# Performance work log

Hardware: AMD Instinct MI355X
Metric: run time of the kernel (lower is better)

Reference implementation:

```python
import jax, jax.numpy as jnp
import numpy as np

EPS = 1e-5
KEEP_FRAC = 0.925


def conv1x1(x, w, b):
    # x: [B,C,H,W], w: [O,C], b: [O]
    return jnp.einsum('bchw,oc->bohw', x, w) + b[None, :, None, None]


def adain_norm(x):
    m = x.mean(axis=(2, 3), keepdims=True)
    v = x.var(axis=(2, 3), keepdims=True)
    return (x - m) / jnp.sqrt(v + EPS)


def zca_norm(x):
    B, C, H, W = x.shape
    f = x.reshape(B, C, H * W)
    m = f.mean(axis=-1, keepdims=True)
    fc = f - m
    cov = jnp.einsum('bcn,bdn->bcd', fc, fc) / (H * W - 1) + EPS * jnp.eye(C, dtype=x.dtype)
    s, U = jnp.linalg.eigh(cov)
    Ud = U * (1.0 / jnp.sqrt(s + EPS))[:, None, :]          # U @ diag(s^-1/2)
    whiten = jnp.einsum('bce,bde->bcd', Ud, U)              # U diag U^T
    out = jnp.einsum('bcd,bdn->bcn', whiten, fc)
    return out.reshape(B, C, H, W)


def correlation_block(xq, yk, wf, bf, wg, bg):
    B, C, H, W = xq.shape
    f = conv1x1(xq, wf, bf).reshape(B, C, -1)   # [B,C,n_x]
    g = conv1x1(yk, wg, bg).reshape(B, C, -1)   # [B,C,n_y]
    energy = jnp.einsum('bcn,bcm->bnm', f, g)   # f^T g : [B,n_x,n_y]
    corr = jax.nn.softmax(energy, axis=-1)
    atten = corr.mean(axis=1, keepdims=True)    # mean over n_x -> [B,1,n_y]
    return corr, atten


def attn_mask(a):
    # a: [B,1,n]; zero the positions of the k smallest values (union over batch, as in torch)
    n = a.shape[2]
    k = int(n * KEEP_FRAC)
    idx = jnp.argsort(a, axis=2)[:, :, :k]                   # smallest k per (b, channel)
    mask = jnp.ones_like(a).at[:, :, idx.reshape(-1)].set(0.0)
    return mask


def corr_mask(mx, my):
    # mx: [B,1,n_x], my: [B,1,n_y] -> equality mask [B,n_x,n_y]
    return (mx[:, 0, :, None] == my[:, 0, None, :]).astype(mx.dtype)


def savanet_forward(x, y, f_w, f_b, g_w, g_b, sa_f_w, sa_f_b, sa_g_w, sa_g_b, h_w, h_b, out_w, out_b):
    B, C, H, W = x.shape
    n = H * W
    x_adain = adain_norm(x)
    y_adain = adain_norm(y)
    x_zca = zca_norm(x)
    y_zca = zca_norm(y)
    correlation, _ = correlation_block(x_adain, y_adain, f_w, f_b, g_w, g_b)
    _, atten_x = correlation_block(x_zca, x_zca, sa_f_w, sa_f_b, sa_g_w, sa_g_b)
    _, atten_y = correlation_block(y_zca, y_zca, sa_f_w, sa_f_b, sa_g_w, sa_g_b)
    mx = attn_mask(atten_x)
    my = attn_mask(atten_y)
    cmask = corr_mask(mx, my)                               # [B,n,n]
    correlation = cmask * correlation
    l1 = jnp.clip(jnp.abs(correlation).sum(axis=2, keepdims=True), 1e-12, None)
    correlation = correlation / l1                          # F.normalize(p=1, dim=2)
    h = conv1x1(y, h_w, h_b).reshape(B, C, n)               # [B,C,n_y]
    residual = jnp.einsum('bcm,bnm->bcn', h, correlation)   # h @ corr^T -> [B,C,n_x]
    residual = residual.reshape(B, C, H, W)
    residual = conv1x1(residual, out_w, out_b)
    output = x + residual
    return output, atten_x, atten_y


def setup_inputs() -> dict:
    key = jax.random.key(0)
    ks = jax.random.split(key, 10)
    B, C, H, W = 2, 512, 64, 64
    scale = 0.02
    d = {
        'x': jax.random.normal(ks[0], (B, C, H, W), dtype=jnp.float32),
        'y': jax.random.normal(ks[1], (B, C, H, W), dtype=jnp.float32),
        'f_w': jax.random.normal(ks[2], (C, C), dtype=jnp.float32) * scale,
        'f_b': jnp.zeros((C,), dtype=jnp.float32),
        'g_w': jax.random.normal(ks[3], (C, C), dtype=jnp.float32) * scale,
        'g_b': jnp.zeros((C,), dtype=jnp.float32),
        'sa_f_w': jax.random.normal(ks[4], (C, C), dtype=jnp.float32) * scale,
        'sa_f_b': jnp.zeros((C,), dtype=jnp.float32),
        'sa_g_w': jax.random.normal(ks[5], (C, C), dtype=jnp.float32) * scale,
        'sa_g_b': jnp.zeros((C,), dtype=jnp.float32),
        'h_w': jax.random.normal(ks[6], (C, C), dtype=jnp.float32) * scale,
        'h_b': jnp.zeros((C,), dtype=jnp.float32),
        'out_w': jax.random.normal(ks[7], (C, C), dtype=jnp.float32) * scale,
        'out_b': jnp.zeros((C,), dtype=jnp.float32),
    }
    return d


def reference(x, y, f_w, f_b, g_w, g_b, sa_f_w, sa_f_b, sa_g_w, sa_g_b, h_w, h_b, out_w, out_b):
    return savanet_forward(x, y, f_w, f_b, g_w, g_b, sa_f_w, sa_f_b, sa_g_w, sa_g_b, h_w, h_b, out_w, out_b)
```

## Files before the change

kernel.cpp:

```cpp
#include <hip/hip_runtime.h>
#include <cstdint>

static constexpr int B2 = 2;
static constexpr int C = 512;
static constexpr int N = 4096;
static constexpr long CN = (long)C * N;
static constexpr long NC = (long)N * C;
static constexpr long CC = (long)C * C;
static constexpr long NN = (long)N * N;
static constexpr float EPSC = 1e-5f;
static constexpr int KSEL = 308;
static constexpr int NS_ITERS = 4;

typedef __attribute__((ext_vector_type(8))) __bf16 bf16x8;
typedef __attribute__((ext_vector_type(4))) float f32x4;

__device__ __forceinline__ float wredSum(float v){
#pragma unroll
  for (int o = 32; o >= 1; o >>= 1) v += __shfl_xor(v, o, 64);
  return v;
}

__device__ __forceinline__ void gld16(const __bf16* g, __bf16* l){
  __builtin_amdgcn_global_load_lds(
      (const __attribute__((address_space(1))) void*)g,
      (__attribute__((address_space(3))) void*)l, 16, 0, 0);
}

__device__ __forceinline__ void splitw(float v, __bf16* ph, __bf16* pl, long o){
  __bf16 h = (__bf16)v;
  ph[o] = h;
  pl[o] = (__bf16)(v - (float)h);
}

template<int PASSES, int TMH, int OUTMODE, int ROWP>
__global__ __launch_bounds__(256) void k_mm(
    const __bf16* __restrict__ Ah, const __bf16* __restrict__ Al,
    const __bf16* __restrict__ Bh, const __bf16* __restrict__ Bl,
    float* __restrict__ Cf, __bf16* __restrict__ Coh, __bf16* __restrict__ Col,
    int Nn, int K, long sAz, long sBz, long sCz,
    float alpha, const float* __restrict__ alpha_ptr,
    const float* __restrict__ brow, long sBr,
    const float* __restrict__ bcol, long sBc,
    const float* __restrict__ c0p,
    const float* __restrict__ addsrc, long sAddz,
    float* __restrict__ Pm, float* __restrict__ Ps, float* __restrict__ Pq,
    const float* __restrict__ mxp, const float* __restrict__ myp)
{
  constexpr int NB = (PASSES == 3) ? 4 : 2;
  constexpr int SB = (PASSES == 3) ? 2 : 1;
  __shared__ __align__(16) __bf16 sm[NB][128 * 32];
  __shared__ float pmx[2][128], psx[2][128], pqx[2][128];
  const int z = blockIdx.z;
  const int nwx = gridDim.x;
  int lin = blockIdx.y * nwx + blockIdx.x;
  const int nwg = nwx * gridDim.y;
  if ((nwg & 7) == 0){
    const int cpx = nwg >> 3;
    lin = (lin & 7) * cpx + (lin >> 3);
  }
  const int i0 = (lin % nwx) * 128;
  const int j0 = (lin / nwx) * 128;
  const int tid = threadIdx.x;
  const int lane = tid & 63;
  const int w = tid >> 6;
  const int wr = (w >> 1) * 64, wc = (w & 1) * 64;
  const int lr = lane & 15;
  const int g = lane >> 4;

  const __bf16* pAh = Ah + (long)z * sAz + (long)i0 * K;
  const __bf16* pBh = Bh + (long)z * sBz + (long)j0 * K;
  const __bf16* pAl = (PASSES == 3) ? (Al + (long)z * sAz + (long)i0 * K) : nullptr;
  const __bf16* pBl = (PASSES == 3) ? (Bl + (long)z * sBz + (long)j0 * K) : nullptr;

  f32x4 acc[4][4] = {};

  for (int kt = 0; kt < K; kt += 32){
#pragma unroll
    for (int p = 0; p < 2; ++p){
      const int t2 = p * 256 + tid;
      const int row = t2 >> 2;
      const int gs = (t2 & 3) ^ ((row >> 1) & 3);
      const long go = (long)row * K + kt + gs * 8;
      gld16(pAh + go, &sm[0][t2 * 8]);
      gld16(pBh + go, &sm[SB][t2 * 8]);
      if constexpr (PASSES == 3){
        gld16(pAl + go, &sm[1][t2 * 8]);
        gld16(pBl + go, &sm[3][t2 * 8]);
      }
    }
    __syncthreads();
    bf16x8 fa[4], fal[4], fb[4], fbl[4];
#pragma unroll
    for (int mi = 0; mi < 4; ++mi){
      const int row = wr + mi * 16 + lr;
      const int off = row * 32 + ((g ^ ((row >> 1) & 3)) * 8);
      fa[mi] = *(const bf16x8*)(&sm[0][off]);
      if constexpr (PASSES == 3) fal[mi] = *(const bf16x8*)(&sm[1][off]);
    }
#pragma unroll
    for (int ni = 0; ni < 4; ++ni){
      const int row = wc + ni * 16 + lr;
      const int off = row * 32 + ((g ^ ((row >> 1) & 3)) * 8);
      fb[ni] = *(const bf16x8*)(&sm[SB][off]);
      if constexpr (PASSES == 3) fbl[ni] = *(const bf16x8*)(&sm[3][off]);
    }
#pragma unroll
    for (int mi = 0; mi < 4; ++mi)
#pragma unroll
      for (int ni = 0; ni < 4; ++ni){
        acc[mi][ni] = __builtin_amdgcn_mfma_f32_16x16x32_bf16(fa[mi], fb[ni], acc[mi][ni], 0, 0, 0);
        if constexpr (PASSES == 3){
          acc[mi][ni] = __builtin_amdgcn_mfma_f32_16x16x32_bf16(fa[mi],  fbl[ni], acc[mi][ni], 0, 0, 0);
          acc[mi][ni] = __builtin_amdgcn_mfma_f32_16x16x32_bf16(fal[mi], fb[ni],  acc[mi][ni], 0, 0, 0);
        }
      }
    __syncthreads();
  }

  float al2 = alpha;
  if (alpha_ptr) al2 *= alpha_ptr[z];
  const float c0v = c0p ? c0p[z] : 0.f;
#pragma unroll
  for (int mi = 0; mi < 4; ++mi){
    float vv[4][4];
    float mrow[4] = {-3.4e38f, -3.4e38f, -3.4e38f, -3.4e38f};
#pragma unroll
    for (int ni = 0; ni < 4; ++ni){
      const int col = j0 + wc + ni * 16 + lr;
      const float bc = (bcol ? bcol[z * sBc + col] : 0.f) + c0v;
#pragma unroll
      for (int j = 0; j < 4; ++j){
        const int row = i0 + wr + mi * 16 + g * 4 + j;
        float v = acc[mi][ni][j] * al2;
        if (TMH) v = (((row == col) ? 3.f : 0.f) - v) * 0.5f;
        if (brow) v += brow[z * sBr + row];
        v += bc;
        if (addsrc) v += addsrc[(long)z * sAddz + (long)row * Nn + col];
        const long o = (long)z * sCz + (long)row * Nn + col;
        if (OUTMODE == 0){ Cf[o] = v; }
        else if (OUTMODE == 1){ __bf16 h = (__bf16)v; Coh[o] = h; Col[o] = (__bf16)(v - (float)h); }
        else { __bf16 h = (__bf16)v; Coh[o] = h; if (ROWP == 2) v = (float)h; }
        if constexpr (ROWP >= 1){
          vv[ni][j] = v;
          mrow[j] = fmaxf(mrow[j], v);
        }
      }
    }
    if constexpr (ROWP >= 1){
#pragma unroll
      for (int j = 0; j < 4; ++j)
#pragma unroll
        for (int o = 1; o <= 8; o <<= 1)
          mrow[j] = fmaxf(mrow[j], __shfl_xor(mrow[j], o, 64));
      float tgt[4];
      if constexpr (ROWP == 2){
#pragma unroll
        for (int j = 0; j < 4; ++j)
          tgt[j] = mxp[i0 + wr + mi * 16 + g * 4 + j];
      }
      float srow[4] = {0.f, 0.f, 0.f, 0.f};
      float qrow[4] = {0.f, 0.f, 0.f, 0.f};
#pragma unroll
      for (int ni = 0; ni < 4; ++ni){
        const float mycol = (ROWP == 2) ? myp[j0 + wc + ni * 16 + lr] : 0.f;
#pragma unroll
        for (int j = 0; j < 4; ++j){
          const float ev = __expf(vv[ni][j] - mrow[j]);
          srow[j] += ev;
          if constexpr (ROWP == 2){
            if (mycol == tgt[j]) qrow[j] += ev;
          }
        }
      }
#pragma unroll
      for (int j = 0; j < 4; ++j){
#pragma unroll
        for (int o = 1; o <= 8; o <<= 1){
          srow[j] += __shfl_xor(srow[j], o, 64);
          if constexpr (ROWP == 2) qrow[j] += __shfl_xor(qrow[j], o, 64);
        }
        if (lr == 0){
          const int rl = wr + mi * 16 + g * 4 + j;
          pmx[w & 1][rl] = mrow[j];
          psx[w & 1][rl] = srow[j];
          if constexpr (ROWP == 2) pqx[w & 1][rl] = qrow[j];
        }
      }
    }
  }
  if constexpr (ROWP >= 1){
    __syncthreads();
    if (tid < 128){
      const float m0 = pmx[0][tid], s0 = psx[0][tid];
      const float m1 = pmx[1][tid], s1 = psx[1][tid];
      const float nm = fmaxf(m0, m1);
      const float c0_ = __expf(m0 - nm), c1_ = __expf(m1 - nm);
      const float s = s0 * c0_ + s1 * c1_;
      const long po = (long)(z * 32 + (j0 >> 7)) * N + i0 + tid;
      Pm[po] = nm;
      Ps[po] = s;
      if constexpr (ROWP == 2){
        Pq[po] = pqx[0][tid] * c0_ + pqx[1][tid] * c1_;
      }
    }
  }
}

template<int TMH, int OUTMODE, int NSYZ>
__global__ __launch_bounds__(256) void k_mm64(
    const __bf16* __restrict__ Ah, const __bf16* __restrict__ Al,
    const __bf16* __restrict__ Bh, const __bf16* __restrict__ Bl,
    const __bf16* __restrict__ tH, const __bf16* __restrict__ tL,
    float* __restrict__ Cf, __bf16* __restrict__ Coh, __bf16* __restrict__ Col,
    int Nn, int K, long sAz, long sBz, long sCz, float alpha)
{
  __shared__ __align__(16) __bf16 sm[4][64 * 64];
  const int z = blockIdx.z;
  const __bf16 *bAh, *bAl, *bBh, *bBl;
  long oC;
  if constexpr (NSYZ){
    if (z < 4){
      bAh = Ah + (long)z * CC; bAl = Al + (long)z * CC;
      bBh = tH + (long)z * CC; bBl = tL + (long)z * CC;
      oC = (long)z * CC;
    } else {
      const int zz = z - 4;
      bAh = tH + (long)zz * CC; bAl = tL + (long)zz * CC;
      bBh = Ah + (long)(4 + zz) * CC; bBl = Al + (long)(4 + zz) * CC;
      oC = (long)(4 + zz) * CC;
    }
  } else {
    bAh = Ah + (long)z * sAz; bAl = Al + (long)z * sAz;
    bBh = Bh + (long)z * sBz; bBl = Bl + (long)z * sBz;
    oC = (long)z * sCz;
  }
  const int i0 = blockIdx.x * 64;
  const int j0 = blockIdx.y * 64;
  const int tid = threadIdx.x;
  const int lane = tid & 63;
  const int w = tid >> 6;
  const int wr = (w >> 1) * 32, wc = (w & 1) * 32;
  const int lr = lane & 15;
  const int g = lane >> 4;

  const __bf16* pAh = bAh + (long)i0 * K;
  const __bf16* pAl = bAl + (long)i0 * K;
  const __bf16* pBh = bBh + (long)j0 * K;
  const __bf16* pBl = bBl + (long)j0 * K;

  f32x4 acc[2][2] = {};

  for (int kt = 0; kt < K; kt += 64){
#pragma unroll
    for (int p = 0; p < 2; ++p){
      const int t2 = p * 256 + tid;
      const int row = t2 >> 3;
      const int gs = (t2 & 7) ^ (row & 7);
      const long go = (long)row * K + kt + gs * 8;
      gld16(pAh + go, &sm[0][t2 * 8]);
      gld16(pAl + go, &sm[1][t2 * 8]);
      gld16(pBh + go, &sm[2][t2 * 8]);
      gld16(pBl + go, &sm[3][t2 * 8]);
    }
    __syncthreads();
#pragma unroll
    for (int ks = 0; ks < 2; ++ks){
      bf16x8 fa[2], fal[2], fb[2], fbl[2];
#pragma unroll
      for (int mi = 0; mi < 2; ++mi){
        const int row = wr + mi * 16 + lr;
        const int off = row * 64 + (((ks * 4 + g) ^ (row & 7)) * 8);
        fa[mi]  = *(const bf16x8*)(&sm[0][off]);
        fal[mi] = *(const bf16x8*)(&sm[1][off]);
      }
#pragma unroll
      for (int ni = 0; ni < 2; ++ni){
        const int row = wc + ni * 16 + lr;
        const int off = row * 64 + (((ks * 4 + g) ^ (row & 7)) * 8);
        fb[ni]  = *(const bf16x8*)(&sm[2][off]);
        fbl[ni] = *(const bf16x8*)(&sm[3][off]);
      }
#pragma unroll
      for (int mi = 0; mi < 2; ++mi)
#pragma unroll
        for (int ni = 0; ni < 2; ++ni){
          acc[mi][ni] = __builtin_amdgcn_mfma_f32_16x16x32_bf16(fa[mi],  fb[ni],  acc[mi][ni], 0, 0, 0);
          acc[mi][ni] = __builtin_amdgcn_mfma_f32_16x16x32_bf16(fa[mi],  fbl[ni], acc[mi][ni], 0, 0, 0);
          acc[mi][ni] = __builtin_amdgcn_mfma_f32_16x16x32_bf16(fal[mi], fb[ni],  acc[mi][ni], 0, 0, 0);
        }
    }
    __syncthreads();
  }

#pragma unroll
  for (int mi = 0; mi < 2; ++mi){
#pragma unroll
    for (int ni = 0; ni < 2; ++ni){
      const int col = j0 + wc + ni * 16 + lr;
#pragma unroll
      for (int j = 0; j < 4; ++j){
        const int row = i0 + wr + mi * 16 + g * 4 + j;
        float v = acc[mi][ni][j] * alpha;
        if (TMH) v = (((row == col) ? 3.f : 0.f) - v) * 0.5f;
        const long o = oC + (long)row * Nn + col;
        if (OUTMODE == 0){ Cf[o] = v; }
        else { __bf16 h = (__bf16)v; Coh[o] = h; Col[o] = (__bf16)(v - (float)h); }
      }
    }
  }
}

__global__ __launch_bounds__(256) void k_pv(
    const __bf16* __restrict__ E, const __bf16* __restrict__ Bh,
    const float* __restrict__ rm, const float* __restrict__ rsc,
    const float* __restrict__ mxv, const float* __restrict__ myv,
    __bf16* __restrict__ resH)
{
  __shared__ __align__(16) __bf16 sa[64 * 64];
  __shared__ __align__(16) __bf16 sb[128 * 64];
  const int z = blockIdx.z;
  int lin = blockIdx.y * 64 + blockIdx.x;
  lin = (lin & 7) * 32 + (lin >> 3);
  const int n0 = (lin & 63) * 64;
  const int c0 = (lin >> 6) * 128;
  const int tid = threadIdx.x;
  const int lane = tid & 63;
  const int w = tid >> 6;
  const int wr = (w >> 1) * 32, wc = (w & 1) * 64;
  const int lr = lane & 15, g = lane >> 4;

  const __bf16* pe = E + (long)z * NN + (long)n0 * N;
  const __bf16* pB = Bh + (long)z * CN + (long)c0 * N;

  const int ar = tid >> 2;
  const int slot = tid & 3;
  const float rmv = rm[(long)z * N + n0 + ar];
  const float rsv = rsc[(long)z * N + n0 + ar];
  const float tgt = mxv[n0 + ar];
  const __bf16* per = pe + (long)ar * N;

  f32x4 acc[2][4] = {};

  for (int kt = 0; kt < N; kt += 64){
#pragma unroll
    for (int d = 0; d < 2; ++d){
      const int gd = slot * 2 + d;
      const bf16x8 ev = *(const bf16x8*)(per + kt + gd * 8);
      const float4 m0 = *(const float4*)(myv + kt + gd * 8);
      const float4 m1 = *(const float4*)(myv + kt + gd * 8 + 4);
      bf16x8 pk;
      pk[0] = (__bf16)((m0.x == tgt) ? __expf((float)ev[0] - rmv) * rsv : 0.f);
      pk[1] = (__bf16)((m0.y == tgt) ? __expf((float)ev[1] - rmv) * rsv : 0.f);
      pk[2] = (__bf16)((m0.z == tgt) ? __expf((float)ev[2] - rmv) * rsv : 0.f);
      pk[3] = (__bf16)((m0.w == tgt) ? __expf((float)ev[3] - rmv) * rsv : 0.f);
      pk[4] = (__bf16)((m1.x == tgt) ? __expf((float)ev[4] - rmv) * rsv : 0.f);
      pk[5] = (__bf16)((m1.y == tgt) ? __expf((float)ev[5] - rmv) * rsv : 0.f);
      pk[6] = (__bf16)((m1.z == tgt) ? __expf((float)ev[6] - rmv) * rsv : 0.f);
      pk[7] = (__bf16)((m1.w == tgt) ? __expf((float)ev[7] - rmv) * rsv : 0.f);
      *(bf16x8*)(&sa[ar * 64 + ((gd ^ (ar & 7)) * 8)]) = pk;
    }
#pragma unroll
    for (int p = 0; p < 4; ++p){
      const int t2 = p * 256 + tid;
      const int row = t2 >> 3;
      const int gs = (t2 & 7) ^ (row & 7);
      gld16(pB + (long)row * N + kt + gs * 8, &sb[t2 * 8]);
    }
    __syncthreads();
#pragma unroll
    for (int ks = 0; ks < 2; ++ks){
      bf16x8 fa[2], fb[4];
#pragma unroll
      for (int mi = 0; mi < 2; ++mi){
        const int row = wr + mi * 16 + lr;
        fa[mi] = *(const bf16x8*)(&sa[row * 64 + (((ks * 4 + g) ^ (row & 7)) * 8)]);
      }
#pragma unroll
      for (int ni = 0; ni < 4; ++ni){
        const int row = wc + ni * 16 + lr;
        fb[ni] = *(const bf16x8*)(&sb[row * 64 + (((ks * 4 + g) ^ (row & 7)) * 8)]);
      }
#pragma unroll
      for (int mi = 0; mi < 2; ++mi)
#pragma unroll
        for (int ni = 0; ni < 4; ++ni)
          acc[mi][ni] = __builtin_amdgcn_mfma_f32_16x16x32_bf16(fa[mi], fb[ni], acc[mi][ni], 0, 0, 0);
    }
    __syncthreads();
  }
#pragma unroll
  for (int mi = 0; mi < 2; ++mi)
#pragma unroll
    for (int ni = 0; ni < 4; ++ni){
      const int c = c0 + wc + ni * 16 + lr;
#pragma unroll
      for (int j = 0; j < 4; ++j){
        const int n = n0 + wr + mi * 16 + g * 4 + j;
        resH[(long)z * NC + (long)n * C + c] = (__bf16)acc[mi][ni][j];
      }
    }
}

__global__ __launch_bounds__(256) void k_wtw(const float* __restrict__ A, const float* __restrict__ B,
                                             float* __restrict__ C2, float alpha){
  __shared__ float sa[16][32], sb[16][32];
  const int i0 = blockIdx.x * 32, j0 = blockIdx.y * 32;
  const int t = threadIdx.x;
  const int ti = t & 15, tj = t >> 4;
  const int li = t & 31, lc = t >> 5;
  float acc[2][2] = {};
  for (int cb = 0; cb < C; cb += 16){
    sa[lc][li]     = A[(long)(cb + lc) * C + i0 + li];
    sa[lc + 8][li] = A[(long)(cb + lc + 8) * C + i0 + li];
    sb[lc][li]     = B[(long)(cb + lc) * C + j0 + li];
    sb[lc + 8][li] = B[(long)(cb + lc + 8) * C + j0 + li];
    __syncthreads();
#pragma unroll
    for (int c = 0; c < 16; ++c){
      const float a0 = sa[c][ti * 2], a1 = sa[c][ti * 2 + 1];
      const float b0 = sb[c][tj * 2], b1 = sb[c][tj * 2 + 1];
      acc[0][0] = fmaf(a0, b0, acc[0][0]); acc[0][1] = fmaf(a0, b1, acc[0][1]);
      acc[1][0] = fmaf(a1, b0, acc[1][0]); acc[1][1] = fmaf(a1, b1, acc[1][1]);
    }
    __syncthreads();
  }
#pragma unroll
  for (int r = 0; r < 2; ++r)
#pragma unroll
    for (int s = 0; s < 2; ++s)
      C2[(long)(i0 + ti * 2 + r) * C + j0 + tj * 2 + s] = acc[r][s] * alpha;
}

__global__ __launch_bounds__(256) void k_wtv(const float* __restrict__ W, const float* __restrict__ b,
                                             float* __restrict__ u){
  __shared__ float sb2[C];
  const int t = threadIdx.x;
  sb2[t] = b[t]; sb2[t + 256] = b[t + 256];
  __syncthreads();
  const int e = blockIdx.x * 256 + t;
  float acc = 0.f;
  for (int c = 0; c < C; ++c) acc = fmaf(W[(long)c * C + e], sb2[c], acc);
  u[e] = acc;
}

__global__ void k_dot2(const float* __restrict__ a1, const float* __restrict__ b1,
                       const float* __restrict__ a2, const float* __restrict__ b2,
                       float* __restrict__ c0m2, float* __restrict__ c0s4){
  const int t = threadIdx.x;
  float s1 = 0.f, s2 = 0.f;
  for (int i = t; i < C; i += 256){ s1 += a1[i] * b1[i]; s2 += a2[i] * b2[i]; }
  __shared__ float sh1[4], sh2[4];
  s1 = wredSum(s1); s2 = wredSum(s2);
  if ((t & 63) == 0){ sh1[t >> 6] = s1; sh2[t >> 6] = s2; }
  __syncthreads();
  if (t == 0){
    float d1 = sh1[0] + sh1[1] + sh1[2] + sh1[3];
    float d2 = sh2[0] + sh2[1] + sh2[2] + sh2[3];
    c0m2[0] = d1; c0m2[1] = d1;
    c0s4[0] = d2; c0s4[1] = d2; c0s4[2] = d2; c0s4[3] = d2;
  }
}

__global__ __launch_bounds__(256) void k_pixvec(const __bf16* __restrict__ X, const float* __restrict__ u,
                                                float* __restrict__ out){
  const int z = blockIdx.y;
  const int wv = threadIdx.x >> 6, lane = threadIdx.x & 63;
  const int n = blockIdx.x * 4 + wv;
  float acc = 0.f;
  for (int d = lane; d < C; d += 64) acc += (float)X[(long)z * NC + (long)n * C + d] * u[d];
  acc = wredSum(acc);
  if (lane == 0) out[(long)z * N + n] = acc;
}

__global__ __launch_bounds__(256) void k_stats(const float* __restrict__ x, const float* __restrict__ y,
                                               float* __restrict__ meanv, float* __restrict__ invs){
  const int bid = blockIdx.x;
  const int t = bid >> 9, c = bid & 511;
  const float* src = (t < 2 ? x : y) + (long)(t & 1) * CN + (long)c * N;
  const int tid = threadIdx.x;
  float s1 = 0.f, s2 = 0.f;
  for (int i = tid; i < N; i += 256){ float v = src[i]; s1 += v; s2 += v * v; }
  __shared__ float sh1[4], sh2[4];
  s1 = wredSum(s1); s2 = wredSum(s2);
  if ((tid & 63) == 0){ sh1[tid >> 6] = s1; sh2[tid >> 6] = s2; }
  __syncthreads();
  if (tid == 0){
    float m = (sh1[0] + sh1[1] + sh1[2] + sh1[3]) * (1.f / (float)N);
    float ex2 = (sh2[0] + sh2[1] + sh2[2] + sh2[3]) * (1.f / (float)N);
    float var = ex2 - m * m;
    meanv[t * C + c] = m;
    invs[t * C + c] = rsqrtf((var > 0.f ? var : 0.f) + EPSC);
  }
}

__global__ __launch_bounds__(256) void k_prep(const float* __restrict__ src,
                                              const float* __restrict__ meanv, const float* __restrict__ invs, int toff,
                                              __bf16* __restrict__ adH,
                                              __bf16* __restrict__ fcH, __bf16* __restrict__ fcL,
                                              __bf16* __restrict__ ccH, __bf16* __restrict__ ccL,
                                              __bf16* __restrict__ rwH){
  __shared__ float tile[64][65];
  const int z = blockIdx.z;
  const int n0 = blockIdx.x * 64;
  const int c0 = blockIdx.y * 64;
  const int tid = threadIdx.x;
  const int tx = tid & 63, ty = tid >> 6;
  const int tgt = toff + z;
#pragma unroll
  for (int it = 0; it < 16; ++it){
    const int cc = it * 4 + ty;
    const float v = src[(long)z * CN + (long)(c0 + cc) * N + n0 + tx];
    tile[cc][tx] = v;
    const float cen = v - meanv[tgt * C + c0 + cc];
    splitw(cen, ccH, ccL, (long)tgt * CN + (long)(c0 + cc) * N + n0 + tx);
  }
  __syncthreads();
  const float m = meanv[tgt * C + c0 + tx];
  const float r = invs[tgt * C + c0 + tx];
#pragma unroll
  for (int it = 0; it < 16; ++it){
    const int p = it * 4 + ty;
    const float v = tile[tx][p];
    const float cen = v - m;
    const long o = (long)z * NC + (long)(n0 + p) * C + c0 + tx;
    adH[o] = (__bf16)(cen * r);
    splitw(cen, fcH, fcL, (long)tgt * NC + (long)(n0 + p) * C + c0 + tx);
    if (rwH) rwH[o] = (__bf16)v;
  }
}

__global__ __launch_bounds__(256) void k_wcvt(const float* __restrict__ s, __bf16* __restrict__ h,
                                              __bf16* __restrict__ l, int n){
  int i = blockIdx.x * 256 + threadIdx.x;
  if (i < n) splitw(s[i], h, l, i);
}
__global__ __launch_bounds__(256) void k_wcvt_h(const float* __restrict__ s, __bf16* __restrict__ h, int n){
  int i = blockIdx.x * 256 + threadIdx.x;
  if (i < n) h[i] = (__bf16)s[i];
}

__global__ void k_diag(float* __restrict__ cov){
  const int z = blockIdx.x, t = threadIdx.x;
  for (int i = t; i < C; i += 256) cov[(long)z * CC + (long)i * C + i] += 2.f * EPSC;
}

__global__ __launch_bounds__(256) void k_powit(const float* __restrict__ cov,
                                               float* __restrict__ invt, float* __restrict__ invsqt){
  __shared__ float v[C], red[4];
  const int z = blockIdx.x, t = threadIdx.x;
  const float* A = cov + (long)z * CC;
  const int j0 = t, j1 = t + 256;
  v[j0] = 1.f + 0.0003f * (float)j0;
  v[j1] = 1.f + 0.0003f * (float)j1;
  __syncthreads();
  float lam = 1.f;
  for (int it = 0; it < 4; ++it){
    float w0a = 0.f, w0b = 0.f, w1a = 0.f, w1b = 0.f;
#pragma unroll 8
    for (int c = 0; c < C; c += 2){
      const float vc0 = v[c], vc1 = v[c + 1];
      w0a = fmaf(A[(long)c * C + j0], vc0, w0a);
      w1a = fmaf(A[(long)c * C + j1], vc0, w1a);
      w0b = fmaf(A[(long)(c + 1) * C + j0], vc1, w0b);
      w1b = fmaf(A[(long)(c + 1) * C + j1], vc1, w1b);
    }
    const float w0 = w0a + w0b, w1 = w1a + w1b;
    float s = w0 * w0 + w1 * w1;
    s = wredSum(s);
    if ((t & 63) == 0) red[t >> 6] = s;
    __syncthreads();
    const float nrm = sqrtf(red[0] + red[1] + red[2] + red[3]);
    lam = nrm;
    const float inv = 1.f / nrm;
    v[j0] = w0 * inv;
    v[j1] = w1 * inv;
    __syncthreads();
  }
  if (t == 0){
    const float tt = 1.02f * lam;
    invt[z] = 1.f / tt;
    invsqt[z] = rsqrtf(tt);
  }
}

__global__ __launch_bounds__(256) void k_ns_init(const float* __restrict__ cov, const float* __restrict__ invt,
                                                 __bf16* __restrict__ h, __bf16* __restrict__ l,
                                                 __bf16* __restrict__ cph, __bf16* __restrict__ cpl){
  const int r = blockIdx.x, z = blockIdx.y;
  const long base = (long)z * CC + (long)r * C;
  const float it = invt[z];
  for (int i = threadIdx.x; i < C; i += 256){
    const float v = cov[base + i] * it;
    splitw(v, h, l, base + i);
    splitw(v, cph, cpl, base + i);
    h[4 * CC + base + i] = (__bf16)((i == r) ? 1.f : 0.f);
    l[4 * CC + base + i] = (__bf16)0.f;
  }
}

__global__ __launch_bounds__(256) void k_prowmerge(const float* __restrict__ Pm, const float* __restrict__ Ps,
                                                   float* __restrict__ rm, float* __restrict__ rsc){
  const int row = blockIdx.x * 256 + threadIdx.x;
  float m = -3.4e38f, s = 0.f;
#pragma unroll 4
  for (int p = 0; p < 32; ++p){
    const float mp = Pm[(long)p * N + row];
    const float sp = Ps[(long)p * N + row];
    const float nm = fmaxf(m, mp);
    s = s * __expf(m - nm) + sp * __expf(mp - nm);
    m = nm;
  }
  rm[row] = m;
  rsc[row] = 1.f / s;
}

__global__ __launch_bounds__(256) void k_prowmerge_m(const float* __restrict__ Pm, const float* __restrict__ Ps,
                                                     const float* __restrict__ Pq,
                                                     float* __restrict__ rm, float* __restrict__ rsc){
  const int z = blockIdx.y;
  const int row = blockIdx.x * 256 + threadIdx.x;
  float m = -3.4e38f, s = 0.f, q = 0.f;
#pragma unroll 4
  for (int p = 0; p < 32; ++p){
    const long idx = (long)(z * 32 + p) * N + row;
    const float mp = Pm[idx], sp = Ps[idx], qp = Pq[idx];
    const float nm = fmaxf(m, mp);
    const float c0_ = __expf(m - nm), c1_ = __expf(mp - nm);
    s = s * c0_ + sp * c1_;
    q = q * c0_ + qp * c1_;
    m = nm;
  }
  float l1 = q / s;
  if (l1 < 1e-12f) l1 = 1e-12f;
  rsc[(long)z * N + row] = 1.f / (s * l1);
  rm[(long)z * N + row] = m;
}

__global__ __launch_bounds__(256) void k_colaccum(const float* __restrict__ E, const float* __restrict__ rowmax,
                                                  const float* __restrict__ rowscale, float* __restrict__ partials){
  const int j = (blockIdx.x * 256 + threadIdx.x) * 4;
  const int r0 = blockIdx.y * 32;
  float4 acc = {0.f, 0.f, 0.f, 0.f};
#pragma unroll 4
  for (int r2 = r0; r2 < r0 + 32; ++r2){
    const float4 e = *reinterpret_cast<const float4*>(E + (long)r2 * N + j);
    const float rmv = rowmax[r2], rsv = rowscale[r2];
    acc.x += __expf(e.x - rmv) * rsv;
    acc.y += __expf(e.y - rmv) * rsv;
    acc.z += __expf(e.z - rmv) * rsv;
    acc.w += __expf(e.w - rmv) * rsv;
  }
  *reinterpret_cast<float4*>(partials + (long)blockIdx.y * N + j) = acc;
}

__global__ __launch_bounds__(256) void k_colreduce(const float* __restrict__ partials, float* __restrict__ att){
  const int j = blockIdx.x * 256 + threadIdx.x;
  float s = 0.f;
#pragma unroll 8
  for (int p = 0; p < 128; ++p) s += partials[(long)p * N + j];
  att[j] = s * (1.f / (float)N);
}

__global__ __launch_bounds__(256) void k_radix(const float* __restrict__ a, float* __restrict__ thr){
  __shared__ unsigned int vals[N];
  __shared__ float shc[4];
  __shared__ unsigned int p_sh;
  __shared__ int k_sh;
  const float* pa = a + (long)blockIdx.x * N;
  const int tid = threadIdx.x;
  for (int i = tid; i < N; i += 256) vals[i] = __float_as_uint(pa[i]);
  if (tid == 0){ p_sh = 0u; k_sh = KSEL; }
  __syncthreads();
  for (int b = 31; b >= 0; --b){
    const unsigned int bit = 1u << b;
    const unsigned int above = (b == 31) ? 0u : ~((bit << 1) - 1u);
    const unsigned int p = p_sh;
    int cnt = 0;
    for (int i = tid; i < N; i += 256){
      unsigned int v = vals[i];
      if ((v & above) == p && (v & bit)) cnt++;
    }
    float cf = wredSum((float)cnt);
    if ((tid & 63) == 0) shc[tid >> 6] = cf;
    __syncthreads();
    if (tid == 0){
      int c1 = (int)(shc[0] + shc[1] + shc[2] + shc[3] + 0.5f);
      if (k_sh <= c1) p_sh = p | bit;
      else k_sh -= c1;
    }
    __syncthreads();
  }
  if (tid == 0) thr[blockIdx.x] = __uint_as_float(p_sh);
}

__global__ __launch_bounds__(256) void k_mask(const float* __restrict__ ax, const float* __restrict__ ay,
                                              const float* __restrict__ thr, float* __restrict__ mx,
                                              float* __restrict__ my){
  int j = blockIdx.x * 256 + threadIdx.x;
  mx[j] = (ax[j] >= thr[0] && ax[N + j] >= thr[1]) ? 1.f : 0.f;
  my[j] = (ay[j] >= thr[2] && ay[N + j] >= thr[3]) ? 1.f : 0.f;
}

extern "C" void kernel_launch(void* const* d_in, const int* in_sizes, int n_in,
                              void* d_out, int out_size, void* d_ws, size_t ws_size,
                              hipStream_t stream)
{
  const float* x     = (const float*)d_in[0];
  const float* y     = (const float*)d_in[1];
  const float* f_w   = (const float*)d_in[2];
  const float* f_b   = (const float*)d_in[3];
  const float* g_w   = (const float*)d_in[4];
  const float* g_b   = (const float*)d_in[5];
  const float* saf_w = (const float*)d_in[6];
  const float* saf_b = (const float*)d_in[7];
  const float* sag_w = (const float*)d_in[8];
  const float* sag_b = (const float*)d_in[9];
  const float* h_w   = (const float*)d_in[10];
  const float* h_b   = (const float*)d_in[11];
  const float* ow    = (const float*)d_in[12];
  const float* ob    = (const float*)d_in[13];

  const size_t MBy = 1ull << 20;
  const size_t KBy = 1ull << 10;
  char* base = (char*)d_ws;
  if (ws_size < 206 * MBy) return;
  auto F  = [&](size_t off){ return (float*)(base + off); };
  auto Bp = [&](size_t off){ return (__bf16*)(base + off); };

  float *E0 = F(0);
  __bf16 *Ebf = Bp(0);
  __bf16 *ccH = Bp(0), *ccL = Bp(16*MBy);
  float  *covb = F(32*MBy);
  __bf16 *zpolH = Bp(36*MBy), *zpolL = Bp(38*MBy);
  __bf16 *covPH = Bp(40*MBy), *covPL = Bp(42*MBy);
  float  *KsTf = F(44*MBy), *K2tf = F(45*MBy);
  __bf16 *KsTH = Bp(46*MBy), *KsTL = Bp(46*MBy + 512*KBy);
  __bf16 *K2tH = Bp(47*MBy), *hwH = Bp(47*MBy + 512*KBy);
  __bf16 *tpH = Bp(48*MBy), *tpL = Bp(50*MBy);
  __bf16 *xaH = Bp(64*MBy);
  __bf16 *xzH = Bp(64*MBy), *xzL = Bp(80*MBy);
  __bf16 *ypmH = Bp(96*MBy);
  __bf16 *AsH = Bp(96*MBy), *AsL = Bp(112*MBy);
  __bf16 *fcH = Bp(128*MBy), *fcL = Bp(144*MBy);
  __bf16 *resH = Bp(128*MBy);
  __bf16 *nsAh = Bp(160*MBy), *nsAl = Bp(164*MBy);
  __bf16 *nsBh = Bp(168*MBy), *nsBl = Bp(172*MBy);
  __bf16 *A2H = Bp(176*MBy);
  __bf16 *yaH = Bp(184*MBy);
  __bf16 *hH  = Bp(192*MBy);
  __bf16 *owH = Bp(200*MBy);
  size_t so = 200 * MBy + 512 * KBy;
  auto SF = [&](size_t bytes){ float* p = F(so); so += bytes; return p; };
  float *meanv = SF(8*KBy), *invs = SF(8*KBy);
  float *rm = SF(32*KBy), *rsc = SF(32*KBy);
  float *mxv = SF(16*KBy), *myv = SF(16*KBy);
  float *rvec2 = SF(32*KBy), *cvec2 = SF(32*KBy);
  float *rvS = SF(64*KBy), *cvS = SF(64*KBy);
  float *u1m = SF(2*KBy), *u2m = SF(2*KBy), *u1s = SF(2*KBy), *u2s = SF(2*KBy);
  float *c0m2 = SF(64), *c0s4 = SF(64), *thr = SF(64);
  float *invt = SF(64), *invsqt = SF(64);
  float *partials = F(201*MBy);
  float *Pm = F(203*MBy);
  float *Ps = F(204*MBy);
  float *Pq = F(205*MBy);

  float* outm = (float*)d_out;
  float* attx = outm + B2 * CN;
  float* atty = attx + (long)B2 * N;

  k_stats<<<dim3(4 * C), dim3(256), 0, stream>>>(x, y, meanv, invs);
  k_prep<<<dim3(64, 8, 2), dim3(256), 0, stream>>>(x, meanv, invs, 0, xaH, fcH, fcL, ccH, ccL, nullptr);
  k_prep<<<dim3(64, 8, 2), dim3(256), 0, stream>>>(y, meanv, invs, 2, yaH, fcH, fcL, ccH, ccL, ypmH);

  k_wtw<<<dim3(16, 16), dim3(256), 0, stream>>>(sag_w, saf_w, KsTf, 1.f);
  k_wtw<<<dim3(16, 16), dim3(256), 0, stream>>>(g_w, f_w, K2tf, 1.f);
  {
    const int nb = (int)(CC / 256);
    k_wcvt<<<nb, 256, 0, stream>>>(KsTf, KsTH, KsTL, (int)CC);
    k_wcvt_h<<<nb, 256, 0, stream>>>(K2tf, K2tH, (int)CC);
    k_wcvt_h<<<nb, 256, 0, stream>>>(h_w, hwH, (int)CC);
    k_wcvt_h<<<nb, 256, 0, stream>>>(ow, owH, (int)CC);
  }
  k_wtv<<<dim3(2), dim3(256), 0, stream>>>(g_w, f_b, u1m);
  k_wtv<<<dim3(2), dim3(256), 0, stream>>>(f_w, g_b, u2m);
  k_wtv<<<dim3(2), dim3(256), 0, stream>>>(sag_w, saf_b, u1s);
  k_wtv<<<dim3(2), dim3(256), 0, stream>>>(saf_w, sag_b, u2s);
  k_dot2<<<dim3(1), dim3(256), 0, stream>>>(f_b, g_b, saf_b, sag_b, c0m2, c0s4);
  k_pixvec<<<dim3(N / 4, 2), dim3(256), 0, stream>>>(xaH, u2m, rvec2);
  k_pixvec<<<dim3(N / 4, 2), dim3(256), 0, stream>>>(yaH, u1m, cvec2);

  k_mm64<0,0,0><<<dim3(8, 8, 4), dim3(256), 0, stream>>>(
      ccH, ccL, ccH, ccL, nullptr, nullptr, covb, nullptr, nullptr, C, N, CN, CN, CC, 1.f / (float)(N - 1));
  k_diag<<<dim3(4), dim3(256), 0, stream>>>(covb);
  k_powit<<<dim3(4), dim3(256), 0, stream>>>(covb, invt, invsqt);

  k_mm<1,0,2,0><<<dim3(32, 4, 2), dim3(256), 0, stream>>>(xaH, nullptr, K2tH, nullptr, nullptr, A2H, nullptr,
      C, C, NC, 0, NC, 1.f, nullptr, nullptr, 0, nullptr, 0, nullptr, nullptr, 0,
      nullptr, nullptr, nullptr, nullptr, nullptr);
  k_mm<1,0,2,0><<<dim3(4, 32, 2), dim3(256), 0, stream>>>(hwH, nullptr, ypmH, nullptr, nullptr, hH, nullptr,
      N, C, 0, NC, CN, 1.f, nullptr, h_b, 0, nullptr, 0, nullptr, nullptr, 0,
      nullptr, nullptr, nullptr, nullptr, nullptr);

  k_ns_init<<<dim3(C, 4), dim3(256), 0, stream>>>(covb, invt, nsAh, nsAl, covPH, covPL);
  __bf16 *cah = nsAh, *cal = nsAl, *cbh = nsBh, *cbl = nsBl;
  for (int it = 0; it < NS_ITERS; ++it){
    k_mm64<1,1,0><<<dim3(8, 8, 4), dim3(256), 0, stream>>>(
        cah + 4*CC, cal + 4*CC, cah, cal, nullptr, nullptr, nullptr, tpH, tpL, C, C, CC, CC, CC, 1.f);
    k_mm64<0,1,1><<<dim3(8, 8, 8), dim3(256), 0, stream>>>(
        cah, cal, nullptr, nullptr, tpH, tpL, nullptr, cbh, cbl, C, C, CC, CC, CC, 1.f);
    __bf16* t;
    t = cah; cah = cbh; cbh = t;
    t = cal; cal = cbl; cbl = t;
  }
  k_mm64<0,1,0><<<dim3(8, 8, 4), dim3(256), 0, stream>>>(
      cah + 4*CC, cal + 4*CC, cah + 4*CC, cal + 4*CC, nullptr, nullptr, nullptr, tpH, tpL, C, C, CC, CC, CC, 1.f);
  k_mm64<1,1,0><<<dim3(8, 8, 4), dim3(256), 0, stream>>>(
      covPH, covPL, tpH, tpL, nullptr, nullptr, nullptr, cbh, cbl, C, C, CC, CC, CC, 1.f);
  k_mm64<0,1,0><<<dim3(8, 8, 4), dim3(256), 0, stream>>>(
      cah + 4*CC, cal + 4*CC, cbh, cbl, nullptr, nullptr, nullptr, zpolH, zpolL, C, C, CC, CC, CC, 1.f);

  k_mm<3,0,1,0><<<dim3(32, 4, 4), dim3(256), 0, stream>>>(fcH, fcL, zpolH, zpolL, nullptr, xzH, xzL,
      C, C, NC, CC, NC, 1.f, invsqt, nullptr, 0, nullptr, 0, nullptr, nullptr, 0,
      nullptr, nullptr, nullptr, nullptr, nullptr);

  k_pixvec<<<dim3(N / 4, 4), dim3(256), 0, stream>>>(xzH, u2s, rvS);
  k_pixvec<<<dim3(N / 4, 4), dim3(256), 0, stream>>>(xzH, u1s, cvS);
  k_mm<3,0,1,0><<<dim3(32, 4, 4), dim3(256), 0, stream>>>(xzH, xzL, KsTH, KsTL, nullptr, AsH, AsL,
      C, C, NC, 0, NC, 1.f, nullptr, nullptr, 0, nullptr, 0, nullptr, nullptr, 0,
      nullptr, nullptr, nullptr, nullptr, nullptr);

  for (int z = 0; z < 4; ++z){
    k_mm<3,0,0,1><<<dim3(32, 32, 1), dim3(256), 0, stream>>>(AsH + (long)z*NC, AsL + (long)z*NC,
        xzH + (long)z*NC, xzL + (long)z*NC, E0, nullptr, nullptr,
        N, C, 0, 0, 0, 1.f, nullptr, rvS + (long)z*N, 0, cvS + (long)z*N, 0, c0s4, nullptr, 0,
        Pm, Ps, nullptr, nullptr, nullptr);
    k_prowmerge<<<dim3(16), dim3(256), 0, stream>>>(Pm, Ps, rm, rsc);
    k_colaccum<<<dim3(4, 128), dim3(256), 0, stream>>>(E0, rm, rsc, partials);
    k_colreduce<<<dim3(16), dim3(256), 0, stream>>>(partials, (z < 2 ? attx : atty) + (long)(z & 1) * N);
  }

  k_radix<<<dim3(2), dim3(256), 0, stream>>>(attx, thr);
  k_radix<<<dim3(2), dim3(256), 0, stream>>>(atty, thr + 2);
  k_mask<<<dim3(16), dim3(256), 0, stream>>>(attx, atty, thr, mxv, myv);

  k_mm<1,0,2,2><<<dim3(32, 32, 2), dim3(256), 0, stream>>>(A2H, nullptr, yaH, nullptr, nullptr, Ebf, nullptr,
      N, C, NC, NC, NN, 1.f, nullptr, rvec2, N, cvec2, N, c0m2, nullptr, 0,
      Pm, Ps, Pq, mxv, myv);
  k_prowmerge_m<<<dim3(16, 2), dim3(256), 0, stream>>>(Pm, Ps, Pq, rm, rsc);
  k_pv<<<dim3(64, 4, 2), dim3(256), 0, stream>>>(Ebf, hH, rm, rsc, mxv, myv, resH);
  k_mm<1,0,0,0><<<dim3(4, 32, 2), dim3(256), 0, stream>>>(owH, nullptr, resH, nullptr, outm, nullptr, nullptr,
      N, C, 0, NC, CN, 1.f, nullptr, ob, 0, nullptr, 0, nullptr, x, CN,
      nullptr, nullptr, nullptr, nullptr, nullptr);
}
```

Baseline: 1.254 ms.

## Fuse small launches, trim the final Newton-Schulz step, and deepen the PV k-tile

Several independent changes. The diagonal epsilon add is folded into the power-iteration and NS-init kernels, so the separate diag kernel is dropped. The two pixel-vector dot passes become one kernel, and the two radix launches become one four-block launch. The last Newton-Schulz iteration computes only the half of the batch that is consumed later. k_pv's K tile grows from 64 to 128 with a 16-way swizzle, which halves its loop trips and barriers but uses more LDS, so occupancy may drop. The merged radix launch relies on atty sitting directly after attx in memory.

```diff
diff --git a/kernel.cpp b/kernel.cpp
--- a/kernel.cpp
+++ b/kernel.cpp
@@ -219,7 +219,7 @@
   const int z = blockIdx.z;
   const __bf16 *bAh, *bAl, *bBh, *bBl;
   long oC;
-  if constexpr (NSYZ){
+  if constexpr (NSYZ == 1){
     if (z < 4){
       bAh = Ah + (long)z * CC; bAl = Al + (long)z * CC;
       bBh = tH + (long)z * CC; bBl = tL + (long)z * CC;
@@ -230,6 +230,10 @@
       bBh = Ah + (long)(4 + zz) * CC; bBl = Al + (long)(4 + zz) * CC;
       oC = (long)(4 + zz) * CC;
     }
+  } else if constexpr (NSYZ == 2){
+    bAh = tH + (long)z * CC; bAl = tL + (long)z * CC;
+    bBh = Ah + (long)(4 + z) * CC; bBl = Al + (long)(4 + z) * CC;
+    oC = (long)(4 + z) * CC;
   } else {
     bAh = Ah + (long)z * sAz; bAl = Al + (long)z * sAz;
     bBh = Bh + (long)z * sBz; bBl = Bl + (long)z * sBz;
@@ -317,8 +321,8 @@
     const float* __restrict__ mxv, const float* __restrict__ myv,
     __bf16* __restrict__ resH)
 {
-  __shared__ __align__(16) __bf16 sa[64 * 64];
-  __shared__ __align__(16) __bf16 sb[128 * 64];
+  __shared__ __align__(16) __bf16 sa[64 * 128];
+  __shared__ __align__(16) __bf16 sb[128 * 128];
   const int z = blockIdx.z;
   int lin = blockIdx.y * 64 + blockIdx.x;
   lin = (lin & 7) * 32 + (lin >> 3);
@@ -342,10 +346,10 @@
 
   f32x4 acc[2][4] = {};
 
-  for (int kt = 0; kt < N; kt += 64){
-#pragma unroll
-    for (int d = 0; d < 2; ++d){
-      const int gd = slot * 2 + d;
+  for (int kt = 0; kt < N; kt += 128){
+#pragma unroll
+    for (int d = 0; d < 4; ++d){
+      const int gd = slot * 4 + d;
       const bf16x8 ev = *(const bf16x8*)(per + kt + gd * 8);
       const float4 m0 = *(const float4*)(myv + kt + gd * 8);
       const float4 m1 = *(const float4*)(myv + kt + gd * 8 + 4);
@@ -358,28 +362,28 @@
       pk[5] = (__bf16)((m1.y == tgt) ? __expf((float)ev[5] - rmv) * rsv : 0.f);
       pk[6] = (__bf16)((m1.z == tgt) ? __expf((float)ev[6] - rmv) * rsv : 0.f);
       pk[7] = (__bf16)((m1.w == tgt) ? __expf((float)ev[7] - rmv) * rsv : 0.f);
-      *(bf16x8*)(&sa[ar * 64 + ((gd ^ (ar & 7)) * 8)]) = pk;
-    }
-#pragma unroll
-    for (int p = 0; p < 4; ++p){
+      *(bf16x8*)(&sa[ar * 128 + ((gd ^ (ar & 15)) * 8)]) = pk;
+    }
+#pragma unroll
+    for (int p = 0; p < 8; ++p){
       const int t2 = p * 256 + tid;
-      const int row = t2 >> 3;
-      const int gs = (t2 & 7) ^ (row & 7);
+      const int row = t2 >> 4;
+      const int gs = (t2 & 15) ^ (row & 15);
       gld16(pB + (long)row * N + kt + gs * 8, &sb[t2 * 8]);
     }
     __syncthreads();
 #pragma unroll
-    for (int ks = 0; ks < 2; ++ks){
+    for (int ks = 0; ks < 4; ++ks){
       bf16x8 fa[2], fb[4];
 #pragma unroll
       for (int mi = 0; mi < 2; ++mi){
         const int row = wr + mi * 16 + lr;
-        fa[mi] = *(const bf16x8*)(&sa[row * 64 + (((ks * 4 + g) ^ (row & 7)) * 8)]);
+        fa[mi] = *(const bf16x8*)(&sa[row * 128 + (((ks * 4 + g) ^ (row & 15)) * 8)]);
       }
 #pragma unroll
       for (int ni = 0; ni < 4; ++ni){
         const int row = wc + ni * 16 + lr;
-        fb[ni] = *(const bf16x8*)(&sb[row * 64 + (((ks * 4 + g) ^ (row & 7)) * 8)]);
+        fb[ni] = *(const bf16x8*)(&sb[row * 128 + (((ks * 4 + g) ^ (row & 15)) * 8)]);
       }
 #pragma unroll
       for (int mi = 0; mi < 2; ++mi)
@@ -471,6 +475,23 @@
   for (int d = lane; d < C; d += 64) acc += (float)X[(long)z * NC + (long)n * C + d] * u[d];
   acc = wredSum(acc);
   if (lane == 0) out[(long)z * N + n] = acc;
+}
+
+__global__ __launch_bounds__(256) void k_pixvec2(const __bf16* __restrict__ X,
+                                                 const float* __restrict__ u1, const float* __restrict__ u2,
+                                                 float* __restrict__ out1, float* __restrict__ out2){
+  const int z = blockIdx.y;
+  const int wv = threadIdx.x >> 6, lane = threadIdx.x & 63;
+  const int n = blockIdx.x * 4 + wv;
+  float a1 = 0.f, a2 = 0.f;
+  for (int d = lane; d < C; d += 64){
+    const float xv = (float)X[(long)z * NC + (long)n * C + d];
+    a1 = fmaf(xv, u1[d], a1);
+    a2 = fmaf(xv, u2[d], a2);
+  }
+  a1 = wredSum(a1);
+  a2 = wredSum(a2);
+  if (lane == 0){ out1[(long)z * N + n] = a1; out2[(long)z * N + n] = a2; }
 }
 
 __global__ __launch_bounds__(256) void k_stats(const float* __restrict__ x, const float* __restrict__ y,
@@ -538,11 +559,6 @@
 __global__ __launch_bounds__(256) void k_wcvt_h(const float* __restrict__ s, __bf16* __restrict__ h, int n){
   int i = blockIdx.x * 256 + threadIdx.x;
   if (i < n) h[i] = (__bf16)s[i];
-}
-
-__global__ void k_diag(float* __restrict__ cov){
-  const int z = blockIdx.x, t = threadIdx.x;
-  for (int i = t; i < C; i += 256) cov[(long)z * CC + (long)i * C + i] += 2.f * EPSC;
 }
 
 __global__ __launch_bounds__(256) void k_powit(const float* __restrict__ cov,
@@ -565,7 +581,8 @@
       w0b = fmaf(A[(long)(c + 1) * C + j0], vc1, w0b);
       w1b = fmaf(A[(long)(c + 1) * C + j1], vc1, w1b);
     }
-    const float w0 = w0a + w0b, w1 = w1a + w1b;
+    const float w0 = w0a + w0b + 2.f * EPSC * v[j0];
+    const float w1 = w1a + w1b + 2.f * EPSC * v[j1];
     float s = w0 * w0 + w1 * w1;
     s = wredSum(s);
     if ((t & 63) == 0) red[t >> 6] = s;
@@ -591,7 +608,8 @@
   const long base = (long)z * CC + (long)r * C;
   const float it = invt[z];
   for (int i = threadIdx.x; i < C; i += 256){
-    const float v = cov[base + i] * it;
+    const float cv = cov[base + i] + ((i == r) ? 2.f * EPSC : 0.f);
+    const float v = cv * it;
     splitw(v, h, l, base + i);
     splitw(v, cph, cpl, base + i);
     h[4 * CC + base + i] = (__bf16)((i == r) ? 1.f : 0.f);
@@ -792,7 +810,6 @@
 
   k_mm64<0,0,0><<<dim3(8, 8, 4), dim3(256), 0, stream>>>(
       ccH, ccL, ccH, ccL, nullptr, nullptr, covb, nullptr, nullptr, C, N, CN, CN, CC, 1.f / (float)(N - 1));
-  k_diag<<<dim3(4), dim3(256), 0, stream>>>(covb);
   k_powit<<<dim3(4), dim3(256), 0, stream>>>(covb, invt, invsqt);
 
   k_mm<1,0,2,0><<<dim3(32, 4, 2), dim3(256), 0, stream>>>(xaH, nullptr, K2tH, nullptr, nullptr, A2H, nullptr,
@@ -807,8 +824,13 @@
   for (int it = 0; it < NS_ITERS; ++it){
     k_mm64<1,1,0><<<dim3(8, 8, 4), dim3(256), 0, stream>>>(
         cah + 4*CC, cal + 4*CC, cah, cal, nullptr, nullptr, nullptr, tpH, tpL, C, C, CC, CC, CC, 1.f);
-    k_mm64<0,1,1><<<dim3(8, 8, 8), dim3(256), 0, stream>>>(
-        cah, cal, nullptr, nullptr, tpH, tpL, nullptr, cbh, cbl, C, C, CC, CC, CC, 1.f);
+    if (it < NS_ITERS - 1){
+      k_mm64<0,1,1><<<dim3(8, 8, 8), dim3(256), 0, stream>>>(
+          cah, cal, nullptr, nullptr, tpH, tpL, nullptr, cbh, cbl, C, C, CC, CC, CC, 1.f);
+    } else {
+      k_mm64<0,1,2><<<dim3(8, 8, 4), dim3(256), 0, stream>>>(
+          cah, cal, nullptr, nullptr, tpH, tpL, nullptr, cbh, cbl, C, C, CC, CC, CC, 1.f);
+    }
     __bf16* t;
     t = cah; cah = cbh; cbh = t;
     t = cal; cal = cbl; cbl = t;
@@ -824,8 +846,7 @@
       C, C, NC, CC, NC, 1.f, invsqt, nullptr, 0, nullptr, 0, nullptr, nullptr, 0,
       nullptr, nullptr, nullptr, nullptr, nullptr);
 
-  k_pixvec<<<dim3(N / 4, 4), dim3(256), 0, stream>>>(xzH, u2s, rvS);
-  k_pixvec<<<dim3(N / 4, 4), dim3(256), 0, stream>>>(xzH, u1s, cvS);
+  k_pixvec2<<<dim3(N / 4, 4), dim3(256), 0, stream>>>(xzH, u2s, u1s, rvS, cvS);
   k_mm<3,0,1,0><<<dim3(32, 4, 4), dim3(256), 0, stream>>>(xzH, xzL, KsTH, KsTL, nullptr, AsH, AsL,
       C, C, NC, 0, NC, 1.f, nullptr, nullptr, 0, nullptr, 0, nullptr, nullptr, 0,
       nullptr, nullptr, nullptr, nullptr, nullptr);
@@ -840,8 +861,7 @@
     k_colreduce<<<dim3(16), dim3(256), 0, stream>>>(partials, (z < 2 ? attx : atty) + (long)(z & 1) * N);
   }
 
-  k_radix<<<dim3(2), dim3(256), 0, stream>>>(attx, thr);
-  k_radix<<<dim3(2), dim3(256), 0, stream>>>(atty, thr + 2);
+  k_radix<<<dim3(4), dim3(256), 0, stream>>>(attx, thr);
   k_mask<<<dim3(16), dim3(256), 0, stream>>>(attx, atty, thr, mxv, myv);
 
   k_mm<1,0,2,2><<<dim3(32, 32, 2), dim3(256), 0, stream>>>(A2H, nullptr, yaH, nullptr, nullptr, Ebf, nullptr,
```

After: 1.242 ms. Within noise of the previous version (-0.9%).
